# Kernel optimization log

Hardware: AMD Instinct MI355X
Metric: run time of the kernel (lower is better)

Reference implementation:

```python
import jax, jax.numpy as jnp
import numpy as np

T, B, F, H, N = 256, 256, 128, 1024, 2


def setup_inputs() -> dict:
    key = jax.random.key(0)
    ks = jax.random.split(key, 12)
    s_in = 1.0 / np.sqrt(H)  # PyTorch LSTM/Linear init scale ~ U(-1/sqrt(H), 1/sqrt(H))
    u = lambda k, shape: jax.random.uniform(k, shape, jnp.float32, -s_in, s_in)
    inp = {
        "x": jax.random.normal(ks[0], (T, B, F), jnp.float32),
        "W_ih0": u(ks[1], (4 * H, F)),
        "W_hh0": u(ks[2], (4 * H, H)),
        "b_ih0": u(ks[3], (4 * H,)),
        "b_hh0": u(ks[4], (4 * H,)),
        "W_ih1": u(ks[5], (4 * H, H)),
        "W_hh1": u(ks[6], (4 * H, H)),
        "b_ih1": u(ks[7], (4 * H,)),
        "b_hh1": u(ks[8], (4 * H,)),
        "W_lin": u(ks[9], (F, H)),
        "b_lin": u(ks[10], (F,)),
        "bs": B,
    }
    return inp


def _lstm_layer(x, W_ih, W_hh, b_ih, b_hh):
    # x: (T, B, in), returns out (T, B, H), (h_T, c_T) each (B, H)
    # Precompute input projections for all timesteps in one big GEMM.
    xW = jnp.einsum('tbf,gf->tbg', x, W_ih) + b_ih + b_hh  # (T, B, 4H)
    h0 = jnp.zeros((x.shape[1], W_hh.shape[1]), x.dtype)

    def step(carry, xw_t):
        h, c = carry
        gates = xw_t + h @ W_hh.T  # (B, 4H); PyTorch gate order i, f, g, o
        i, f, g, o = jnp.split(gates, 4, axis=-1)
        c = jax.nn.sigmoid(f) * c + jax.nn.sigmoid(i) * jnp.tanh(g)
        h = jax.nn.sigmoid(o) * jnp.tanh(c)
        return (h, c), h

    (h_T, c_T), out = jax.lax.scan(step, (h0, h0), xW)
    return out, h_T, c_T


def reference(x, W_ih0, W_hh0, b_ih0, b_hh0, W_ih1, W_hh1, b_ih1, b_hh1, W_lin, b_lin, bs):
    # Stacked 2-layer LSTM with zero initial state (self.h is None on fresh call).
    out0, h0_T, c0_T = _lstm_layer(x, W_ih0, W_hh0, b_ih0, b_hh0)
    out1, h1_T, c1_T = _lstm_layer(out0, W_ih1, W_hh1, b_ih1, b_hh1)
    # Original: y = linear(out[0]) -> first timestep of top layer output.
    y = out1[0] @ W_lin.T + b_lin  # (B, F)
    h_n = jnp.stack([h0_T, h1_T])  # (N, B, H)
    c_n = jnp.stack([c0_T, c1_T])  # (N, B, H)
    return y, h_n, c_n
```

## Files before the change

### kernel.cpp

```cpp
#include <hip/hip_runtime.h>
#include <stdint.h>


typedef __bf16 bf16x8 __attribute__((ext_vector_type(8)));
typedef float  f32x4  __attribute__((ext_vector_type(4)));
typedef unsigned short ushort8v __attribute__((ext_vector_type(8)));
typedef unsigned short ushort4v __attribute__((ext_vector_type(4)));
typedef unsigned int   uint4v   __attribute__((ext_vector_type(4)));
typedef __attribute__((address_space(1))) unsigned int as1_u32;
typedef __attribute__((address_space(3))) unsigned int as3_u32;

#define T_STEPS 256
#define BATCH   256
#define HDIM    1024
#define GDIM    4096
#define FDIM    128
#define AS_STRIDE 2096

static __device__ __forceinline__ float bf2f(unsigned short u) {
  union { unsigned int i; float f; } v; v.i = ((unsigned int)u) << 16; return v.f;
}
static __device__ __forceinline__ unsigned short f2bf(float f) {
  return __builtin_bit_cast(unsigned short, (__bf16)f);
}
static __device__ __forceinline__ float sigm(float x) { return 1.f / (1.f + __expf(-x)); }
static __device__ __forceinline__ float tanh_f(float x) { return 2.f / (1.f + __expf(-2.f * x)) - 1.f; }

static __device__ __forceinline__ void vl1_inv() {
  asm volatile("buffer_inv" ::: "memory");
}

__global__ void conv_bf16(const float* __restrict__ s, unsigned short* __restrict__ d, int n) {
  int i = blockIdx.x * 256 + threadIdx.x;
  if (i < n) d[i] = f2bf(s[i]);
}

__global__ void diag_kernel(float* out, int n, float v) {
  int i = blockIdx.x * 256 + threadIdx.x;
  if (i < n) out[i] = v;
}

__device__ __forceinline__ void grp_arrive(unsigned int* gbar, bool fast) {
  __syncthreads();
  if (threadIdx.x == 0) {
    if (!fast) __builtin_amdgcn_fence(__ATOMIC_RELEASE, "agent");
    unsigned int my = __hip_atomic_fetch_add(&gbar[0], 1u, __ATOMIC_RELAXED, __HIP_MEMORY_SCOPE_AGENT);
    if ((my & 31u) == 31u)
      __hip_atomic_fetch_add(&gbar[32], 1u, __ATOMIC_RELAXED, __HIP_MEMORY_SCOPE_AGENT);
  }
}

__device__ __forceinline__ void grp_wait_w0(unsigned int* gbar, unsigned int target, bool fast, int wv) {
  if (wv == 0) {
    for (unsigned int it = 0; it < (1u << 14); ++it) {
      unsigned int g = __hip_atomic_load(&gbar[32], __ATOMIC_RELAXED, __HIP_MEMORY_SCOPE_AGENT);
      if ((int)(g - target) >= 0) break;
      __builtin_amdgcn_s_sleep(1);
    }
    if (!fast) __builtin_amdgcn_fence(__ATOMIC_ACQUIRE, "agent");
  }
  __syncthreads();
  if (fast) vl1_inv();
}

__device__ __forceinline__ void grp_barrier(unsigned int* gbar, unsigned int target, bool fast, int wv) {
  grp_arrive(gbar, fast);
  grp_wait_w0(gbar, target, fast, wv);
}

__global__ __launch_bounds__(256) void gemm_bt_xw(
    const unsigned short* __restrict__ A,
    const unsigned short* __restrict__ B,
    unsigned short* __restrict__ xw,
    int K)
{
  const int tid = threadIdx.x, lane = tid & 63, w = tid >> 6;
  const int m0 = blockIdx.x * 128;
  const int n0 = blockIdx.y * 128;
  __shared__ unsigned short As[128 * 64];
  __shared__ unsigned short Bs[128 * 64];
  const int mrow0 = (w & 1) * 64, ncol0 = (w >> 1) * 64;
  const int quad = lane >> 4;

  f32x4 acc[4][4];
  #pragma unroll
  for (int i = 0; i < 4; ++i)
    #pragma unroll
    for (int j = 0; j < 4; ++j) acc[i][j] = f32x4{0.f, 0.f, 0.f, 0.f};

  const int kiter = K >> 6;
  for (int ki = 0; ki < kiter; ++ki) {
    const int k0 = ki * 64;
    __syncthreads();
    #pragma unroll
    for (int i = 0; i < 4; ++i) {
      int obase = (w * 4 + i) * 1024;
      int o = obase + lane * 16;
      int row = o >> 7; int kb = o & 127;
      const char* ga = (const char*)A + ((size_t)(m0 + row) * K + k0) * 2 + kb;
      const char* gb = (const char*)B + ((size_t)(n0 + row) * K + k0) * 2 + kb;
      __builtin_amdgcn_global_load_lds((const as1_u32*)ga, (as3_u32*)((char*)As + obase), 16, 0, 0);
      __builtin_amdgcn_global_load_lds((const as1_u32*)gb, (as3_u32*)((char*)Bs + obase), 16, 0, 0);
    }
    __syncthreads();
    #pragma unroll
    for (int kk = 0; kk < 2; ++kk) {
      bf16x8 af[4], bfr[4];
      #pragma unroll
      for (int mt = 0; mt < 4; ++mt)
        af[mt] = *(const bf16x8*)(As + (mrow0 + mt * 16 + (lane & 15)) * 64 + kk * 32 + quad * 8);
      #pragma unroll
      for (int nt = 0; nt < 4; ++nt)
        bfr[nt] = *(const bf16x8*)(Bs + (ncol0 + nt * 16 + (lane & 15)) * 64 + kk * 32 + quad * 8);
      #pragma unroll
      for (int mt = 0; mt < 4; ++mt)
        #pragma unroll
        for (int nt = 0; nt < 4; ++nt)
          acc[mt][nt] = __builtin_amdgcn_mfma_f32_16x16x32_bf16(af[mt], bfr[nt], acc[mt][nt], 0, 0, 0);
    }
  }
  #pragma unroll
  for (int mt = 0; mt < 4; ++mt) {
    int m = m0 + mrow0 + mt * 16 + quad * 4;
    int tl = m >> 8, b = m & 255;
    #pragma unroll
    for (int nt = 0; nt < 4; ++nt) {
      int col = n0 + ncol0 + nt * 16 + (lane & 15);
      ushort4v v;
      v.x = f2bf(acc[mt][nt][0]); v.y = f2bf(acc[mt][nt][1]);
      v.z = f2bf(acc[mt][nt][2]); v.w = f2bf(acc[mt][nt][3]);
      *(ushort4v*)(xw + ((size_t)tl * GDIM + col) * BATCH + b) = v;
    }
  }
}

__device__ __forceinline__ bool probe_fast(unsigned int* probe, unsigned int* gbar,
                                           unsigned int salt, unsigned int target,
                                           unsigned int* flagLds, int wv) {
  const int wg = blockIdx.x, mi = wg & 7;
  if (threadIdx.x == 0) probe[wg * 32] = salt ^ (unsigned int)wg;
  grp_barrier(gbar, target, true, wv);
  if (threadIdx.x == 0) {
    unsigned int bad = 0;
    for (int k = 0; k < 32; ++k) {
      int member = mi + 8 * k;
      unsigned int v = probe[member * 32];
      if (v != (salt ^ (unsigned int)member)) bad = 1;
    }
    *flagLds = bad;
  }
  __syncthreads();
  return (*flagLds == 0);
}

__global__ __launch_bounds__(1024, 4) void lstm_layer0_kernel(
    const unsigned short* __restrict__ xbf,
    const float* __restrict__ Wih,
    const float* __restrict__ Whh,
    const float* __restrict__ bih,
    const float* __restrict__ bhh,
    unsigned short* __restrict__ slab,
    unsigned short* __restrict__ hx,
    float* __restrict__ cstate,
    int t0, int ch_len, unsigned int gen_base,
    float* __restrict__ dout_h,
    float* __restrict__ dout_c,
    unsigned int* __restrict__ bar,
    unsigned int* __restrict__ probe)
{
  const int tid = threadIdx.x, lane = tid & 63, wv = tid >> 6;
  const int quad = lane >> 4, l15 = lane & 15;
  const int g = wv & 3, kq = wv >> 2;
  const int wg = blockIdx.x;
  const int mi = wg & 7, ni = wg >> 3;
  const int r0 = mi * 32, hc0 = ni * 32;
  unsigned int* gbar = bar + mi * 64;

  __shared__ unsigned short As[32 * (AS_STRIDE / 2)];
  __shared__ float gbuf[16][32][33];
  __shared__ unsigned int flagLds;

  bf16x8 whh[2][8];
  #pragma unroll
  for (int nt = 0; nt < 2; ++nt) {
    const float* wrow = Whh + (size_t)(g * HDIM + hc0 + nt * 16 + l15) * HDIM + kq * 256 + quad * 8;
    #pragma unroll
    for (int kk = 0; kk < 8; ++kk) {
      f32x4 f0 = *(const f32x4*)(wrow + kk * 32);
      f32x4 f1 = *(const f32x4*)(wrow + kk * 32 + 4);
      bf16x8 r;
      r[0] = (__bf16)f0[0]; r[1] = (__bf16)f0[1]; r[2] = (__bf16)f0[2]; r[3] = (__bf16)f0[3];
      r[4] = (__bf16)f1[0]; r[5] = (__bf16)f1[1]; r[6] = (__bf16)f1[2]; r[7] = (__bf16)f1[3];
      whh[nt][kk] = r;
    }
  }
  bf16x8 wih[2];
  #pragma unroll
  for (int nt = 0; nt < 2; ++nt) {
    const float* wrow = Wih + (size_t)(g * HDIM + hc0 + nt * 16 + l15) * FDIM + kq * 32 + quad * 8;
    f32x4 f0 = *(const f32x4*)(wrow);
    f32x4 f1 = *(const f32x4*)(wrow + 4);
    bf16x8 r;
    r[0] = (__bf16)f0[0]; r[1] = (__bf16)f0[1]; r[2] = (__bf16)f0[2]; r[3] = (__bf16)f0[3];
    r[4] = (__bf16)f1[0]; r[5] = (__bf16)f1[1]; r[6] = (__bf16)f1[2]; r[7] = (__bf16)f1[3];
    wih[nt] = r;
  }

  const int hcl = tid & 31, row = tid >> 5;
  float bias[4];
  #pragma unroll
  for (int b4 = 0; b4 < 4; ++b4)
    bias[b4] = bih[b4 * HDIM + hc0 + hcl] + bhh[b4 * HDIM + hc0 + hcl];

  float c1 = (t0 == 0) ? 0.f : cstate[(size_t)(r0 + row) * HDIM + hc0 + hcl];

  unsigned int salt = 0x9E3779B9u ^ (gen_base * 2654435761u);
  bool fast = probe_fast(probe, gbar, salt, gen_base + 1u, &flagLds, wv);

  const int tend = t0 + ch_len;

  f32x4 acc[2][2];
  #pragma unroll
  for (int mt = 0; mt < 2; ++mt)
    #pragma unroll
    for (int nt = 0; nt < 2; ++nt) acc[mt][nt] = f32x4{0.f, 0.f, 0.f, 0.f};
  {
    bf16x8 af[2];
    #pragma unroll
    for (int mt = 0; mt < 2; ++mt)
      af[mt] = *(const bf16x8*)(xbf + (size_t)(t0 * BATCH + r0 + mt * 16 + l15) * FDIM + kq * 32 + quad * 8);
    #pragma unroll
    for (int mt = 0; mt < 2; ++mt)
      #pragma unroll
      for (int nt = 0; nt < 2; ++nt)
        acc[mt][nt] = __builtin_amdgcn_mfma_f32_16x16x32_bf16(af[mt], wih[nt], acc[mt][nt], 0, 0, 0);
  }

  #pragma unroll 1
  for (int t = t0; t < tend; ++t) {
    if (t > 0) {
      const unsigned short* Aprev = hx + (size_t)((t - 1) & 1) * (BATCH * HDIM);
      #pragma unroll
      for (int p = 0; p < 4; ++p) {
        int idx = p * 16 + wv;
        int arow = idx >> 1, half = idx & 1;
        const char* gsrc = (const char*)(Aprev + (size_t)(r0 + arow) * HDIM + half * 512) + lane * 16;
        char* ldst = (char*)As + arow * AS_STRIDE + half * 1024;
        __builtin_amdgcn_global_load_lds((const as1_u32*)gsrc, (as3_u32*)ldst, 16, 0, 0);
      }
      __syncthreads();
      #pragma unroll
      for (int j = 0; j < 8; ++j) {
        bf16x8 af[2];
        #pragma unroll
        for (int mt = 0; mt < 2; ++mt)
          af[mt] = *(const bf16x8*)((const char*)As + (mt * 16 + l15) * AS_STRIDE + kq * 512 + j * 64 + quad * 16);
        #pragma unroll
        for (int mt = 0; mt < 2; ++mt)
          #pragma unroll
          for (int nt = 0; nt < 2; ++nt)
            acc[mt][nt] = __builtin_amdgcn_mfma_f32_16x16x32_bf16(af[mt], whh[nt][j], acc[mt][nt], 0, 0, 0);
      }
    }

    __syncthreads();
    #pragma unroll
    for (int mt = 0; mt < 2; ++mt)
      #pragma unroll
      for (int nt = 0; nt < 2; ++nt) {
        int hl = nt * 16 + l15;
        int rq = mt * 16 + quad * 4;
        #pragma unroll
        for (int i = 0; i < 4; ++i)
          gbuf[wv][hl][rq + i] = acc[mt][nt][i];
      }
    __syncthreads();

    unsigned short* hdst = slab + (size_t)(t - t0 + 1) * (BATCH * HDIM);
    unsigned short* hxd  = hx + (size_t)(t & 1) * (BATCH * HDIM);
    {
      float gi = gbuf[0][hcl][row] + gbuf[4][hcl][row] + gbuf[8][hcl][row]  + gbuf[12][hcl][row] + bias[0];
      float gf = gbuf[1][hcl][row] + gbuf[5][hcl][row] + gbuf[9][hcl][row]  + gbuf[13][hcl][row] + bias[1];
      float gg = gbuf[2][hcl][row] + gbuf[6][hcl][row] + gbuf[10][hcl][row] + gbuf[14][hcl][row] + bias[2];
      float go = gbuf[3][hcl][row] + gbuf[7][hcl][row] + gbuf[11][hcl][row] + gbuf[15][hcl][row] + bias[3];
      float iv = sigm(gi), fv = sigm(gf), gv = tanh_f(gg), ov = sigm(go);
      float cn = fv * c1 + iv * gv;
      c1 = cn;
      float hv = ov * tanh_f(cn);
      int gidx = (r0 + row) * HDIM + hc0 + hcl;
      unsigned short hb = f2bf(hv);
      hxd[gidx] = hb;
      hdst[gidx] = hb;
      if (t == tend - 1) cstate[gidx] = cn;
      if (t == T_STEPS - 1) { dout_h[gidx] = hv; dout_c[gidx] = cn; }
    }

    if (t != tend - 1) {
      grp_arrive(gbar, fast);
      #pragma unroll
      for (int mt = 0; mt < 2; ++mt)
        #pragma unroll
        for (int nt = 0; nt < 2; ++nt) acc[mt][nt] = f32x4{0.f, 0.f, 0.f, 0.f};
      {
        bf16x8 af[2];
        #pragma unroll
        for (int mt = 0; mt < 2; ++mt)
          af[mt] = *(const bf16x8*)(xbf + (size_t)((t + 1) * BATCH + r0 + mt * 16 + l15) * FDIM + kq * 32 + quad * 8);
        #pragma unroll
        for (int mt = 0; mt < 2; ++mt)
          #pragma unroll
          for (int nt = 0; nt < 2; ++nt)
            acc[mt][nt] = __builtin_amdgcn_mfma_f32_16x16x32_bf16(af[mt], wih[nt], acc[mt][nt], 0, 0, 0);
      }
      grp_wait_w0(gbar, gen_base + 2u + (unsigned int)(t - t0), fast, wv);
    }
  }
}

__global__ __launch_bounds__(1024, 4) void lstm_layer1_kernel(
    const unsigned short* __restrict__ xw,
    const float* __restrict__ Whh,
    const float* __restrict__ bih,
    const float* __restrict__ bhh,
    unsigned short* __restrict__ hpp,
    float* __restrict__ cstate,
    int t0, int ch_len, unsigned int gen_base,
    unsigned short* __restrict__ h1t0,
    float* __restrict__ dout_h,
    float* __restrict__ dout_c,
    unsigned int* __restrict__ bar,
    unsigned int* __restrict__ probe)
{
  const int tid = threadIdx.x, lane = tid & 63, wv = tid >> 6;
  const int quad = lane >> 4, l15 = lane & 15;
  const int g = wv & 3, kq = wv >> 2;
  const int wg = blockIdx.x;
  const int mi = wg & 7, ni = wg >> 3;
  const int r0 = mi * 32, hc0 = ni * 32;
  unsigned int* gbar = bar + mi * 64;

  __shared__ unsigned short As[32 * (AS_STRIDE / 2)];
  __shared__ float gbuf[16][32][33];
  __shared__ unsigned int flagLds;

  bf16x8 whh[2][8];
  #pragma unroll
  for (int nt = 0; nt < 2; ++nt) {
    const float* wrow = Whh + (size_t)(g * HDIM + hc0 + nt * 16 + l15) * HDIM + kq * 256 + quad * 8;
    #pragma unroll
    for (int kk = 0; kk < 8; ++kk) {
      f32x4 f0 = *(const f32x4*)(wrow + kk * 32);
      f32x4 f1 = *(const f32x4*)(wrow + kk * 32 + 4);
      bf16x8 r;
      r[0] = (__bf16)f0[0]; r[1] = (__bf16)f0[1]; r[2] = (__bf16)f0[2]; r[3] = (__bf16)f0[3];
      r[4] = (__bf16)f1[0]; r[5] = (__bf16)f1[1]; r[6] = (__bf16)f1[2]; r[7] = (__bf16)f1[3];
      whh[nt][kk] = r;
    }
  }

  const int hcl = tid & 31, row = tid >> 5;
  float bias[4];
  #pragma unroll
  for (int b4 = 0; b4 < 4; ++b4)
    bias[b4] = bih[b4 * HDIM + hc0 + hcl] + bhh[b4 * HDIM + hc0 + hcl];

  float c1 = (t0 == 0) ? 0.f : cstate[(size_t)(r0 + row) * HDIM + hc0 + hcl];

  unsigned int salt = 0xB5297A4Du ^ (gen_base * 2654435761u);
  bool fast = probe_fast(probe, gbar, salt, gen_base + 1u, &flagLds, wv);

  const int tend = t0 + ch_len;

  float xwv[4];
  #pragma unroll
  for (int g4 = 0; g4 < 4; ++g4) {
    const unsigned short* xp =
        xw + ((size_t)0 * GDIM + g4 * HDIM + hc0 + hcl) * BATCH + r0 + row;
    xwv[g4] = bf2f(*xp);
  }

  #pragma unroll 1
  for (int t = t0; t < tend; ++t) {
    f32x4 acc[2][2];
    #pragma unroll
    for (int mt = 0; mt < 2; ++mt)
      #pragma unroll
      for (int nt = 0; nt < 2; ++nt) acc[mt][nt] = f32x4{0.f, 0.f, 0.f, 0.f};

    if (t > 0) {
      const unsigned short* Aprev = hpp + (size_t)((t - 1) & 1) * (BATCH * HDIM);
      #pragma unroll
      for (int p = 0; p < 4; ++p) {
        int idx = p * 16 + wv;
        int arow = idx >> 1, half = idx & 1;
        const char* gsrc = (const char*)(Aprev + (size_t)(r0 + arow) * HDIM + half * 512) + lane * 16;
        char* ldst = (char*)As + arow * AS_STRIDE + half * 1024;
        __builtin_amdgcn_global_load_lds((const as1_u32*)gsrc, (as3_u32*)ldst, 16, 0, 0);
      }
      __syncthreads();
      #pragma unroll
      for (int j = 0; j < 8; ++j) {
        bf16x8 af[2];
        #pragma unroll
        for (int mt = 0; mt < 2; ++mt)
          af[mt] = *(const bf16x8*)((const char*)As + (mt * 16 + l15) * AS_STRIDE + kq * 512 + j * 64 + quad * 16);
        #pragma unroll
        for (int mt = 0; mt < 2; ++mt)
          #pragma unroll
          for (int nt = 0; nt < 2; ++nt)
            acc[mt][nt] = __builtin_amdgcn_mfma_f32_16x16x32_bf16(af[mt], whh[nt][j], acc[mt][nt], 0, 0, 0);
      }
    }

    __syncthreads();
    #pragma unroll
    for (int mt = 0; mt < 2; ++mt)
      #pragma unroll
      for (int nt = 0; nt < 2; ++nt) {
        int hl = nt * 16 + l15;
        int rq = mt * 16 + quad * 4;
        #pragma unroll
        for (int i = 0; i < 4; ++i)
          gbuf[wv][hl][rq + i] = acc[mt][nt][i];
      }
    __syncthreads();

    unsigned short* hdst = hpp + (size_t)(t & 1) * (BATCH * HDIM);
    {
      float gi = gbuf[0][hcl][row] + gbuf[4][hcl][row] + gbuf[8][hcl][row]  + gbuf[12][hcl][row] + xwv[0] + bias[0];
      float gf = gbuf[1][hcl][row] + gbuf[5][hcl][row] + gbuf[9][hcl][row]  + gbuf[13][hcl][row] + xwv[1] + bias[1];
      float gg = gbuf[2][hcl][row] + gbuf[6][hcl][row] + gbuf[10][hcl][row] + gbuf[14][hcl][row] + xwv[2] + bias[2];
      float go = gbuf[3][hcl][row] + gbuf[7][hcl][row] + gbuf[11][hcl][row] + gbuf[15][hcl][row] + xwv[3] + bias[3];
      float iv = sigm(gi), fv = sigm(gf), gv = tanh_f(gg), ov = sigm(go);
      float cn = fv * c1 + iv * gv;
      c1 = cn;
      float hv = ov * tanh_f(cn);
      int gidx = (r0 + row) * HDIM + hc0 + hcl;
      hdst[gidx] = f2bf(hv);
      if (h1t0 != nullptr && t == 0) h1t0[gidx] = f2bf(hv);
      if (t == tend - 1) cstate[gidx] = cn;
      if (t == T_STEPS - 1) { dout_h[gidx] = hv; dout_c[gidx] = cn; }
    }

    if (t != tend - 1) {
      grp_arrive(gbar, fast);
      #pragma unroll
      for (int g4 = 0; g4 < 4; ++g4) {
        const unsigned short* xp =
            xw + ((size_t)(t + 1 - t0) * GDIM + g4 * HDIM + hc0 + hcl) * BATCH + r0 + row;
        xwv[g4] = bf2f(*xp);
      }
      grp_wait_w0(gbar, gen_base + 2u + (unsigned int)(t - t0), fast, wv);
    }
  }
}

__global__ void y_kernel(const unsigned short* __restrict__ h1t0,
                         const unsigned short* __restrict__ wlin,
                         const float* __restrict__ blin,
                         float* __restrict__ y)
{
  int b = blockIdx.x;
  int f = threadIdx.x;
  const ushort8v* hp = (const ushort8v*)(h1t0 + (size_t)b * HDIM);
  const ushort8v* wp = (const ushort8v*)(wlin + (size_t)f * HDIM);
  float acc = 0.f;
  for (int i = 0; i < HDIM / 8; ++i) {
    ushort8v hv = hp[i], wvv = wp[i];
    #pragma unroll
    for (int j = 0; j < 8; ++j) acc += bf2f(hv[j]) * bf2f(wvv[j]);
  }
  y[b * FDIM + f] = acc + blin[f];
}

extern "C" void kernel_launch(void* const* d_in, const int* in_sizes, int n_in,
                              void* d_out, int out_size, void* d_ws, size_t ws_size,
                              hipStream_t stream) {
  (void)in_sizes; (void)n_in; (void)out_size;
  const float* x    = (const float*)d_in[0];
  const float* Wih0 = (const float*)d_in[1];
  const float* Whh0 = (const float*)d_in[2];
  const float* bih0 = (const float*)d_in[3];
  const float* bhh0 = (const float*)d_in[4];
  const float* Wih1 = (const float*)d_in[5];
  const float* Whh1 = (const float*)d_in[6];
  const float* bih1 = (const float*)d_in[7];
  const float* bhh1 = (const float*)d_in[8];
  const float* Wlin = (const float*)d_in[9];
  const float* blin = (const float*)d_in[10];
  float* out = (float*)d_out;

  const size_t SZ_BAR   = 4096;
  const size_t SZ_PROBE = 32768;
  const size_t SZ_XBF   = (size_t)T_STEPS * BATCH * FDIM * 2;
  const size_t SZ_WIH1  = (size_t)GDIM * HDIM * 2;
  const size_t SZ_WLIN  = (size_t)FDIM * HDIM * 2;
  const size_t SZ_HPP   = (size_t)2 * BATCH * HDIM * 2;
  const size_t SZ_HX    = (size_t)2 * BATCH * HDIM * 2;
  const size_t SZ_H1T0  = (size_t)BATCH * HDIM * 2;
  const size_t SZ_CST   = (size_t)BATCH * HDIM * 4;
  const size_t SLOT     = (size_t)BATCH * HDIM * 2;
  const size_t fixed = SZ_BAR + SZ_PROBE + SZ_XBF + SZ_WIH1 + SZ_WLIN + SZ_HPP + SZ_HX + SZ_H1T0 + 2 * SZ_CST;

  int CH = 0;
  const int cands[5] = {64, 32, 16, 8, 4};
  for (int i = 0; i < 5; ++i) {
    int c = cands[i];
    size_t need = fixed + (size_t)(c + 1) * SLOT + (size_t)c * GDIM * BATCH * 2;
    if (need <= ws_size) { CH = c; break; }
  }
  if (CH == 0) {
    float v = 1.0e6f + (float)(ws_size >> 20);
    diag_kernel<<<(32768 + 255) / 256, 256, 0, stream>>>(out, 32768, v);
    return;
  }

  char* ws = (char*)d_ws;
  size_t o = 0;
  unsigned int*   bar   = (unsigned int*)(ws + o);    o += SZ_BAR;
  unsigned int*   probe = (unsigned int*)(ws + o);    o += SZ_PROBE;
  unsigned short* xbf   = (unsigned short*)(ws + o);  o += SZ_XBF;
  unsigned short* wih1b = (unsigned short*)(ws + o);  o += SZ_WIH1;
  unsigned short* wlinb = (unsigned short*)(ws + o);  o += SZ_WLIN;
  unsigned short* h1pp  = (unsigned short*)(ws + o);  o += SZ_HPP;
  unsigned short* hx0   = (unsigned short*)(ws + o);  o += SZ_HX;
  unsigned short* h1t0  = (unsigned short*)(ws + o);  o += SZ_H1T0;
  float*          c0st  = (float*)(ws + o);           o += SZ_CST;
  float*          c1st  = (float*)(ws + o);           o += SZ_CST;
  unsigned short* slab  = (unsigned short*)(ws + o);  o += (size_t)(CH + 1) * SLOT;
  unsigned short* xw1   = (unsigned short*)(ws + o);  o += (size_t)CH * GDIM * BATCH * 2;

  hipMemsetAsync(bar, 0, SZ_BAR, stream);

  conv_bf16<<<(T_STEPS * BATCH * FDIM + 255) / 256, 256, 0, stream>>>(x, xbf, T_STEPS * BATCH * FDIM);
  conv_bf16<<<(GDIM * HDIM + 255) / 256, 256, 0, stream>>>(Wih1, wih1b, GDIM * HDIM);
  conv_bf16<<<(FDIM * HDIM + 255) / 256, 256, 0, stream>>>(Wlin, wlinb, FDIM * HDIM);

  float* hn0 = out + 32768;
  float* hn1 = out + 32768 + 262144;
  float* cn0 = out + 32768 + 524288;
  float* cn1 = out + 32768 + 524288 + 262144;

  unsigned int gen_base = 0;
  for (int ch = 0; ch < T_STEPS / CH; ++ch) {
    int t0 = ch * CH;
    lstm_layer0_kernel<<<256, 1024, 0, stream>>>(
        xbf, Wih0, Whh0, bih0, bhh0, slab, hx0, c0st, t0, CH, gen_base, hn0, cn0, bar, probe);
    gen_base += (unsigned int)CH;
    gemm_bt_xw<<<dim3(CH * 2, 32), 256, 0, stream>>>(
        slab + BATCH * HDIM, wih1b, xw1, HDIM);
    lstm_layer1_kernel<<<256, 1024, 0, stream>>>(
        xw1, Whh1, bih1, bhh1, h1pp, c1st, t0, CH, gen_base, h1t0, hn1, cn1, bar, probe);
    gen_base += (unsigned int)CH;
  }

  y_kernel<<<256, 128, 0, stream>>>(h1t0, wlinb, blin, out);
}
```

Baseline: 3.956 ms.

## Replace group counter barrier with per-block stamps and chunked dataflow h copy

Swaps the shared atomic counter barrier among the 32 workgroups of each row group for per-workgroup generation stamps. In the fast path, each wave polls only the two producer stamps it needs and copies those 32-column h chunks into LDS as soon as they are ready. The per-step async global-to-LDS load moves into the wait phase, so data fetch overlaps with waiting on slower producers, and the LDS row stride is adjusted. This adds more polling traffic (each wave spins on a stamp) and needs extra syncthreads, and ordering correctness now depends on per-stamp release and acquire.

New measurement: 4.654 ms. 17.6% more time.

```diff
diff --git a/kernel.cpp b/kernel.cpp
--- a/kernel.cpp
+++ b/kernel.cpp
@@ -15,7 +15,7 @@
 #define HDIM    1024
 #define GDIM    4096
 #define FDIM    128
-#define AS_STRIDE 2096
+#define AS_STRIDE 2080
 
 static __device__ __forceinline__ float bf2f(unsigned short u) {
   union { unsigned int i; float f; } v; v.i = ((unsigned int)u) << 16; return v.f;
@@ -40,32 +40,27 @@
   if (i < n) out[i] = v;
 }
 
-__device__ __forceinline__ void grp_arrive(unsigned int* gbar, bool fast) {
-  __syncthreads();
-  if (threadIdx.x == 0) {
-    if (!fast) __builtin_amdgcn_fence(__ATOMIC_RELEASE, "agent");
-    unsigned int my = __hip_atomic_fetch_add(&gbar[0], 1u, __ATOMIC_RELAXED, __HIP_MEMORY_SCOPE_AGENT);
-    if ((my & 31u) == 31u)
-      __hip_atomic_fetch_add(&gbar[32], 1u, __ATOMIC_RELAXED, __HIP_MEMORY_SCOPE_AGENT);
-  }
-}
-
-__device__ __forceinline__ void grp_wait_w0(unsigned int* gbar, unsigned int target, bool fast, int wv) {
-  if (wv == 0) {
-    for (unsigned int it = 0; it < (1u << 14); ++it) {
-      unsigned int g = __hip_atomic_load(&gbar[32], __ATOMIC_RELAXED, __HIP_MEMORY_SCOPE_AGENT);
-      if ((int)(g - target) >= 0) break;
-      __builtin_amdgcn_s_sleep(1);
-    }
-    if (!fast) __builtin_amdgcn_fence(__ATOMIC_ACQUIRE, "agent");
-  }
-  __syncthreads();
-  if (fast) vl1_inv();
-}
-
-__device__ __forceinline__ void grp_barrier(unsigned int* gbar, unsigned int target, bool fast, int wv) {
-  grp_arrive(gbar, fast);
-  grp_wait_w0(gbar, target, fast, wv);
+__device__ __forceinline__ void post_stamp(unsigned int* st, unsigned int gen, bool fast) {
+  if (!fast) __builtin_amdgcn_fence(__ATOMIC_RELEASE, "agent");
+  __hip_atomic_store(st, gen, __ATOMIC_RELAXED, __HIP_MEMORY_SCOPE_AGENT);
+}
+__device__ __forceinline__ void poll_ge(unsigned int* st, unsigned int target) {
+  for (unsigned int it = 0; it < (1u << 15); ++it) {
+    unsigned int g = __hip_atomic_load(st, __ATOMIC_RELAXED, __HIP_MEMORY_SCOPE_AGENT);
+    if ((int)(g - target) >= 0) return;
+    if (it > 64) __builtin_amdgcn_s_sleep(1);
+  }
+}
+
+__device__ __forceinline__ void copy_chunk(const unsigned short* __restrict__ src,
+                                           char* AsB, int r0, int ni2, int lane) {
+  int rlo = lane >> 2, cp = lane & 3;
+  const unsigned short* s0 = src + (size_t)(r0 + rlo) * HDIM + ni2 * 32 + cp * 8;
+  uint4v a = *(const uint4v*)(s0);
+  uint4v b = *(const uint4v*)(s0 + 16 * HDIM);
+  char* d0 = AsB + rlo * AS_STRIDE + ni2 * 64 + cp * 16;
+  *(uint4v*)(d0) = a;
+  *(uint4v*)(d0 + 16 * AS_STRIDE) = b;
 }
 
 __global__ __launch_bounds__(256) void gemm_bt_xw(
@@ -134,17 +129,21 @@
   }
 }
 
-__device__ __forceinline__ bool probe_fast(unsigned int* probe, unsigned int* gbar,
-                                           unsigned int salt, unsigned int target,
-                                           unsigned int* flagLds, int wv) {
-  const int wg = blockIdx.x, mi = wg & 7;
-  if (threadIdx.x == 0) probe[wg * 32] = salt ^ (unsigned int)wg;
-  grp_barrier(gbar, target, true, wv);
-  if (threadIdx.x == 0) {
+__device__ __forceinline__ bool probe_chk(unsigned int* probeBuf, unsigned int* stamps,
+                                          unsigned int salt, unsigned int target,
+                                          unsigned int* flagLds) {
+  const int wg = blockIdx.x, mi = wg & 7, ni = wg >> 3;
+  const int tid = threadIdx.x;
+  if (tid == 0) probeBuf[wg * 32] = salt ^ (unsigned int)wg;
+  __syncthreads();
+  if (tid == 0) {
+    __hip_atomic_store(&stamps[ni], target, __ATOMIC_RELAXED, __HIP_MEMORY_SCOPE_AGENT);
+    for (int k = 0; k < 32; ++k) poll_ge(&stamps[k], target);
+    vl1_inv();
     unsigned int bad = 0;
     for (int k = 0; k < 32; ++k) {
       int member = mi + 8 * k;
-      unsigned int v = probe[member * 32];
+      unsigned int v = probeBuf[member * 32];
       if (v != (salt ^ (unsigned int)member)) bad = 1;
     }
     *flagLds = bad;
@@ -174,7 +173,7 @@
   const int wg = blockIdx.x;
   const int mi = wg & 7, ni = wg >> 3;
   const int r0 = mi * 32, hc0 = ni * 32;
-  unsigned int* gbar = bar + mi * 64;
+  unsigned int* stamps = bar + mi * 32;
 
   __shared__ unsigned short As[32 * (AS_STRIDE / 2)];
   __shared__ float gbuf[16][32][33];
@@ -215,10 +214,15 @@
   float c1 = (t0 == 0) ? 0.f : cstate[(size_t)(r0 + row) * HDIM + hc0 + hcl];
 
   unsigned int salt = 0x9E3779B9u ^ (gen_base * 2654435761u);
-  bool fast = probe_fast(probe, gbar, salt, gen_base + 1u, &flagLds, wv);
+  bool fast = probe_chk(probe, stamps, salt, gen_base + 1u, &flagLds);
 
   const int tend = t0 + ch_len;
 
+  if (t0 > 0) {
+    const unsigned short* hsrc = hx + (size_t)((t0 - 1) & 1) * (BATCH * HDIM);
+    copy_chunk(hsrc, (char*)As, r0, wv * 2, lane);
+    copy_chunk(hsrc, (char*)As, r0, wv * 2 + 1, lane);
+  }
   f32x4 acc[2][2];
   #pragma unroll
   for (int mt = 0; mt < 2; ++mt)
@@ -235,20 +239,11 @@
       for (int nt = 0; nt < 2; ++nt)
         acc[mt][nt] = __builtin_amdgcn_mfma_f32_16x16x32_bf16(af[mt], wih[nt], acc[mt][nt], 0, 0, 0);
   }
+  __syncthreads();
 
   #pragma unroll 1
   for (int t = t0; t < tend; ++t) {
     if (t > 0) {
-      const unsigned short* Aprev = hx + (size_t)((t - 1) & 1) * (BATCH * HDIM);
-      #pragma unroll
-      for (int p = 0; p < 4; ++p) {
-        int idx = p * 16 + wv;
-        int arow = idx >> 1, half = idx & 1;
-        const char* gsrc = (const char*)(Aprev + (size_t)(r0 + arow) * HDIM + half * 512) + lane * 16;
-        char* ldst = (char*)As + arow * AS_STRIDE + half * 1024;
-        __builtin_amdgcn_global_load_lds((const as1_u32*)gsrc, (as3_u32*)ldst, 16, 0, 0);
-      }
-      __syncthreads();
       #pragma unroll
       for (int j = 0; j < 8; ++j) {
         bf16x8 af[2];
@@ -263,7 +258,6 @@
       }
     }
 
-    __syncthreads();
     #pragma unroll
     for (int mt = 0; mt < 2; ++mt)
       #pragma unroll
@@ -294,9 +288,12 @@
       if (t == tend - 1) cstate[gidx] = cn;
       if (t == T_STEPS - 1) { dout_h[gidx] = hv; dout_c[gidx] = cn; }
     }
+    __syncthreads();
 
     if (t != tend - 1) {
-      grp_arrive(gbar, fast);
+      const unsigned int tgt = gen_base + 2u + (unsigned int)(t - t0);
+      if (tid == 0) post_stamp(&stamps[ni], tgt, fast);
+
       #pragma unroll
       for (int mt = 0; mt < 2; ++mt)
         #pragma unroll
@@ -312,7 +309,26 @@
           for (int nt = 0; nt < 2; ++nt)
             acc[mt][nt] = __builtin_amdgcn_mfma_f32_16x16x32_bf16(af[mt], wih[nt], acc[mt][nt], 0, 0, 0);
       }
-      grp_wait_w0(gbar, gen_base + 2u + (unsigned int)(t - t0), fast, wv);
+
+      const unsigned short* hsrc = hx + (size_t)(t & 1) * (BATCH * HDIM);
+      if (fast) {
+        #pragma unroll
+        for (int cc = 0; cc < 2; ++cc) {
+          int ni2 = wv * 2 + cc;
+          poll_ge(&stamps[ni2], tgt);
+          vl1_inv();
+          copy_chunk(hsrc, (char*)As, r0, ni2, lane);
+        }
+      } else {
+        if (tid == 0) {
+          for (int j = 0; j < 32; ++j) poll_ge(&stamps[j], tgt);
+          __builtin_amdgcn_fence(__ATOMIC_ACQUIRE, "agent");
+        }
+        __syncthreads();
+        copy_chunk(hsrc, (char*)As, r0, wv * 2, lane);
+        copy_chunk(hsrc, (char*)As, r0, wv * 2 + 1, lane);
+      }
+      __syncthreads();
     }
   }
 }
@@ -337,7 +353,7 @@
   const int wg = blockIdx.x;
   const int mi = wg & 7, ni = wg >> 3;
   const int r0 = mi * 32, hc0 = ni * 32;
-  unsigned int* gbar = bar + mi * 64;
+  unsigned int* stamps = bar + mi * 32;
 
   __shared__ unsigned short As[32 * (AS_STRIDE / 2)];
   __shared__ float gbuf[16][32][33];
@@ -367,10 +383,15 @@
   float c1 = (t0 == 0) ? 0.f : cstate[(size_t)(r0 + row) * HDIM + hc0 + hcl];
 
   unsigned int salt = 0xB5297A4Du ^ (gen_base * 2654435761u);
-  bool fast = probe_fast(probe, gbar, salt, gen_base + 1u, &flagLds, wv);
+  bool fast = probe_chk(probe, stamps, salt, gen_base + 1u, &flagLds);
 
   const int tend = t0 + ch_len;
 
+  if (t0 > 0) {
+    const unsigned short* hsrc = hpp + (size_t)((t0 - 1) & 1) * (BATCH * HDIM);
+    copy_chunk(hsrc, (char*)As, r0, wv * 2, lane);
+    copy_chunk(hsrc, (char*)As, r0, wv * 2 + 1, lane);
+  }
   float xwv[4];
   #pragma unroll
   for (int g4 = 0; g4 < 4; ++g4) {
@@ -378,6 +399,7 @@
         xw + ((size_t)0 * GDIM + g4 * HDIM + hc0 + hcl) * BATCH + r0 + row;
     xwv[g4] = bf2f(*xp);
   }
+  __syncthreads();
 
   #pragma unroll 1
   for (int t = t0; t < tend; ++t) {
@@ -388,16 +410,6 @@
       for (int nt = 0; nt < 2; ++nt) acc[mt][nt] = f32x4{0.f, 0.f, 0.f, 0.f};
 
     if (t > 0) {
-      const unsigned short* Aprev = hpp + (size_t)((t - 1) & 1) * (BATCH * HDIM);
-      #pragma unroll
-      for (int p = 0; p < 4; ++p) {
-        int idx = p * 16 + wv;
-        int arow = idx >> 1, half = idx & 1;
-        const char* gsrc = (const char*)(Aprev + (size_t)(r0 + arow) * HDIM + half * 512) + lane * 16;
-        char* ldst = (char*)As + arow * AS_STRIDE + half * 1024;
-        __builtin_amdgcn_global_load_lds((const as1_u32*)gsrc, (as3_u32*)ldst, 16, 0, 0);
-      }
-      __syncthreads();
       #pragma unroll
       for (int j = 0; j < 8; ++j) {
         bf16x8 af[2];
@@ -412,7 +424,6 @@
       }
     }
 
-    __syncthreads();
     #pragma unroll
     for (int mt = 0; mt < 2; ++mt)
       #pragma unroll
@@ -441,16 +452,38 @@
       if (t == tend - 1) cstate[gidx] = cn;
       if (t == T_STEPS - 1) { dout_h[gidx] = hv; dout_c[gidx] = cn; }
     }
+    __syncthreads();
 
     if (t != tend - 1) {
-      grp_arrive(gbar, fast);
+      const unsigned int tgt = gen_base + 2u + (unsigned int)(t - t0);
+      if (tid == 0) post_stamp(&stamps[ni], tgt, fast);
+
       #pragma unroll
       for (int g4 = 0; g4 < 4; ++g4) {
         const unsigned short* xp =
             xw + ((size_t)(t + 1 - t0) * GDIM + g4 * HDIM + hc0 + hcl) * BATCH + r0 + row;
         xwv[g4] = bf2f(*xp);
       }
-      grp_wait_w0(gbar, gen_base + 2u + (unsigned int)(t - t0), fast, wv);
+
+      const unsigned short* hsrc = hpp + (size_t)(t & 1) * (BATCH * HDIM);
+      if (fast) {
+        #pragma unroll
+        for (int cc = 0; cc < 2; ++cc) {
+          int ni2 = wv * 2 + cc;
+          poll_ge(&stamps[ni2], tgt);
+          vl1_inv();
+          copy_chunk(hsrc, (char*)As, r0, ni2, lane);
+        }
+      } else {
+        if (tid == 0) {
+          for (int j = 0; j < 32; ++j) poll_ge(&stamps[j], tgt);
+          __builtin_amdgcn_fence(__ATOMIC_ACQUIRE, "agent");
+        }
+        __syncthreads();
+        copy_chunk(hsrc, (char*)As, r0, wv * 2, lane);
+        copy_chunk(hsrc, (char*)As, r0, wv * 2 + 1, lane);
+      }
+      __syncthreads();
     }
   }
 }
```
